# Kernel tuning notes

Measured on AMD Instinct MI355X. Metric: run time of the kernel, lower is better.

## Reference

```python
import jax, jax.numpy as jnp
import numpy as np

# ---- static problem configuration (matches init_kwargs) ----
N_PAIRS = 256
NODES_PER_GRAPH = 64
EDGES_PER_GRAPH = 200
MAX_EDGES = 256            # max_edge_set_size
N_GRAPHS = 2 * N_PAIRS     # query/corpus interleaved
N_NODES = N_GRAPHS * NODES_PER_GRAPH
N_EDGES = N_GRAPHS * EDGES_PER_GRAPH
NODE_DIM = 16
EDGE_DIM = 16
H = 128                    # node_state_dim
E_ENC = 64                 # encoded edge feature dim
MSG = 256                  # edge_hidden_sizes[-1] = 2*H (GMN GRU convention)
SK = 32                    # sinkhorn_feature_dim
PROP_STEPS = 5
SK_ITERS = 20
TEMP = 0.1


def setup_inputs() -> dict:
    key = jax.random.key(0)
    ks = jax.random.split(key, 16)
    node_features = jax.random.normal(ks[0], (N_NODES, NODE_DIM), jnp.float32)
    edge_features = jax.random.normal(ks[1], (N_EDGES, EDGE_DIM), jnp.float32)
    # edges are grouped per graph (graph g owns edges [g*E, (g+1)*E)) and
    # endpoints stay inside graph g's node range, as get_graph_features assumes
    offs = np.repeat(np.arange(N_GRAPHS) * NODES_PER_GRAPH, EDGES_PER_GRAPH)
    rng = np.random.default_rng(0)
    from_idx = jnp.asarray(offs + rng.integers(0, NODES_PER_GRAPH, N_EDGES), jnp.int32)
    to_idx = jnp.asarray(offs + rng.integers(0, NODES_PER_GRAPH, N_EDGES), jnp.int32)

    def lin(k, i, o):
        return jax.random.normal(k, (i, o), jnp.float32) / np.sqrt(i).astype(np.float32)

    p = dict(
        enc_node_w=lin(ks[2], NODE_DIM, H), enc_node_b=jnp.zeros((H,), jnp.float32),
        enc_edge_w=lin(ks[3], EDGE_DIM, E_ENC), enc_edge_b=jnp.zeros((E_ENC,), jnp.float32),
        msg_w1=lin(ks[4], 2 * H + E_ENC, MSG), msg_b1=jnp.zeros((MSG,), jnp.float32),
        msg_w2=lin(ks[5], MSG, MSG), msg_b2=jnp.zeros((MSG,), jnp.float32),
        rmsg_w1=lin(ks[6], 2 * H + E_ENC, MSG), rmsg_b1=jnp.zeros((MSG,), jnp.float32),
        rmsg_w2=lin(ks[7], MSG, MSG), rmsg_b2=jnp.zeros((MSG,), jnp.float32),
        gru_w_ih=lin(ks[8], MSG, 3 * H), gru_b_ih=jnp.zeros((3 * H,), jnp.float32),
        gru_w_hh=lin(ks[9], H, 3 * H), gru_b_hh=jnp.zeros((3 * H,), jnp.float32),
        sk_w1=lin(ks[10], MSG, SK), sk_b1=jnp.zeros((SK,), jnp.float32),
        sk_w2=lin(ks[11], SK, SK), sk_b2=jnp.zeros((SK,), jnp.float32),
    )
    return {"node_features": node_features, "edge_features": edge_features,
            "from_idx": from_idx, "to_idx": to_idx, **p}


def _mlp2(x, w1, b1, w2, b2):
    # Linear -> ReLU -> Linear (GMN MLP: no activation after last layer)
    return jax.nn.relu(x @ w1 + b1) @ w2 + b2


def reference(node_features, edge_features, from_idx, to_idx,
              enc_node_w, enc_node_b, enc_edge_w, enc_edge_b,
              msg_w1, msg_b1, msg_w2, msg_b2,
              rmsg_w1, rmsg_b1, rmsg_w2, rmsg_b2,
              gru_w_ih, gru_b_ih, gru_w_hh, gru_b_hh,
              sk_w1, sk_b1, sk_w2, sk_b2):
    # ---- GraphEncoder (single-layer MLPs) ----
    h = node_features @ enc_node_w + enc_node_b          # [N_NODES, H]
    e = edge_features @ enc_edge_w + enc_edge_b          # [N_EDGES, E_ENC]

    def edge_msgs(h):
        s, d = h[from_idx], h[to_idx]                    # gathers [N_EDGES, H]
        fwd = _mlp2(jnp.concatenate([s, d, e], axis=1), msg_w1, msg_b1, msg_w2, msg_b2)
        rev = _mlp2(jnp.concatenate([d, s, e], axis=1), rmsg_w1, rmsg_b1, rmsg_w2, rmsg_b2)
        return fwd, rev                                  # [N_EDGES, MSG] each

    # ---- propagation loop: gather -> edge MLP -> scatter -> GRU update ----
    for _ in range(PROP_STEPS):
        fwd, rev = edge_msgs(h)
        agg = (jax.ops.segment_sum(fwd, to_idx, num_segments=N_NODES)
               + jax.ops.segment_sum(rev, from_idx, num_segments=N_NODES))  # [N_NODES, MSG]
        gi = agg @ gru_w_ih + gru_b_ih                   # [N_NODES, 3H]
        gh = h @ gru_w_hh + gru_b_hh
        r = jax.nn.sigmoid(gi[:, :H] + gh[:, :H])
        z = jax.nn.sigmoid(gi[:, H:2 * H] + gh[:, H:2 * H])
        n = jnp.tanh(gi[:, 2 * H:] + r * gh[:, 2 * H:])
        h = (1.0 - z) * n + z * h                        # torch GRU update

    # ---- propagation_messages: per-edge fwd + rev message ----
    fwd, rev = edge_msgs(h)
    e_final = fwd + rev                                  # [N_EDGES, MSG]

    # ---- split_and_stack: per-graph edge sets padded to MAX_EDGES ----
    stacked = jnp.pad(e_final.reshape(N_GRAPHS, EDGES_PER_GRAPH, MSG),
                      ((0, 0), (0, MAX_EDGES - EDGES_PER_GRAPH), (0, 0)))
    q, c = stacked[0::2], stacked[1::2]                  # [B, MAX_EDGES, MSG]

    # ---- sinkhorn feature MLP + size mask ----
    tq = _mlp2(q, sk_w1, sk_b1, sk_w2, sk_b2)            # [B, MAX_EDGES, SK]
    tc = _mlp2(c, sk_w1, sk_b1, sk_w2, sk_b2)
    mask = (jnp.arange(MAX_EDGES) < EDGES_PER_GRAPH).astype(jnp.float32)[None, :, None]
    mq, mc = mask * tq, mask * tc

    # ---- log-domain Sinkhorn ----
    la = jnp.einsum('bif,bjf->bij', mq, mc) / TEMP       # [B, MAX_EDGES, MAX_EDGES]
    for _ in range(SK_ITERS):
        la = la - jax.nn.logsumexp(la, axis=2, keepdims=True)
        la = la - jax.nn.logsumexp(la, axis=1, keepdims=True)
    plan = jnp.exp(la)

    # ---- feature_alignment_score: -sum relu(q - P @ c) ----
    return -jnp.sum(jax.nn.relu(q - jnp.einsum('bij,bjf->bif', plan, c)), axis=(1, 2))
```

## Files before the change

kernel.cpp:

```cpp
#include <hip/hip_runtime.h>
#include <math.h>

typedef __attribute__((ext_vector_type(4))) float f32x4;
typedef __attribute__((ext_vector_type(8))) short s16x8;
typedef __attribute__((ext_vector_type(4))) short s16x4;

#define NN 32768
#define NE 102400
#define HD 128
#define EED 64
#define MSGD 256
#define NG 512
#define EPG 200
#define NP 256
#define SKD 32

__device__ inline short f2bf(float x){
  union{float f; unsigned u;} z; z.f=x;
  unsigned r = (z.u + 0x7fffu + ((z.u>>16)&1u)) >> 16;
  return (short)r;
}
__device__ inline float bf2f(unsigned short u){
  union{unsigned u; float f;} z; z.u = ((unsigned)u)<<16; return z.f;
}
__device__ inline float frcp(float x){
  float r; asm("v_rcp_f32 %0, %1" : "=v"(r) : "v"(x)); return r;
}

__global__ void __launch_bounds__(256) k_enc_node(const float* __restrict__ nf,
    const float* __restrict__ W, const float* __restrict__ b,
    float* __restrict__ h, short* __restrict__ hb){
  __shared__ float Ws[16*128];
  int t = threadIdx.x;
  for (int i=t;i<16*128;i+=256) Ws[i]=W[i];
  __syncthreads();
  int node = blockIdx.x*2 + (t>>7);
  int f = t & 127;
  const float* x = nf + node*16;
  float acc = b[f];
  #pragma unroll
  for (int k=0;k<16;k++) acc = fmaf(x[k], Ws[k*128+f], acc);
  h[node*HD+f] = acc;
  hb[node*HD+f] = f2bf(acc);
}

__global__ void __launch_bounds__(256) k_enc_edge(const float* __restrict__ ef,
    const float* __restrict__ W, const float* __restrict__ b, short* __restrict__ eeb){
  __shared__ float Ws[16*64];
  int t = threadIdx.x;
  for (int i=t;i<16*64;i+=256) Ws[i]=W[i];
  __syncthreads();
  int edge = blockIdx.x*4 + (t>>6);
  int f = t & 63;
  const float* x = ef + edge*16;
  float acc = b[f];
  #pragma unroll
  for (int k=0;k<16;k++) acc = fmaf(x[k], Ws[k*64+f], acc);
  eeb[edge*EED+f] = f2bf(acc);
}

__global__ void __launch_bounds__(256) k_pack(const float* __restrict__ W,
    short* __restrict__ dst, int K, int N){
  int NT = N >> 4;
  int i = blockIdx.x*256 + threadIdx.x;
  if (i >= (K/32)*NT*64) return;
  int l = i & 63, tile = i >> 6;
  int nt = tile % NT, kt = tile / NT;
  int lr = l & 15, lq = l >> 4;
  s16x8 v;
  #pragma unroll
  for (int j=0;j<8;j++)
    v[j] = f2bf(W[(size_t)(kt*32 + lq*8 + j)*N + nt*16 + lr]);
  *((s16x8*)dst + i) = v;
}

__global__ void __launch_bounds__(256) k_csr_count(const int* __restrict__ fidx,
    const int* __restrict__ tidx, int* __restrict__ cur_in, int* __restrict__ cur_out){
  int e = blockIdx.x*256 + threadIdx.x;
  if (e >= NE) return;
  atomicAdd(&cur_in[tidx[e]], 1);
  atomicAdd(&cur_out[fidx[e]], 1);
}
__global__ void k_csr_scan(int* __restrict__ cur_in, int* __restrict__ start_in,
    int* __restrict__ cur_out, int* __restrict__ start_out){
  if (threadIdx.x) return;
  int g = blockIdx.x;
  int n0 = g*64, base = g*EPG;
  int run = base;
  for (int i=0;i<64;i++){ int c=cur_in[n0+i]; start_in[n0+i]=run; cur_in[n0+i]=run; run+=c; }
  run = base;
  for (int i=0;i<64;i++){ int c=cur_out[n0+i]; start_out[n0+i]=run; cur_out[n0+i]=run; run+=c; }
}
__global__ void __launch_bounds__(256) k_csr_fill(const int* __restrict__ fidx,
    const int* __restrict__ tidx, int* __restrict__ cur_in, int* __restrict__ cur_out,
    int* __restrict__ list_in, int* __restrict__ list_out){
  int e = blockIdx.x*256 + threadIdx.x;
  if (e >= NE) return;
  int p1 = atomicAdd(&cur_in[tidx[e]], 1);  list_in[p1] = e;
  int p2 = atomicAdd(&cur_out[fidx[e]], 1); list_out[p2] = e;
}

__global__ void __launch_bounds__(256,2) k_msg_both(const short* __restrict__ hb,
    const short* __restrict__ eeb, const int* __restrict__ from_idx, const int* __restrict__ to_idx,
    const short* __restrict__ w1f, const float* __restrict__ b1f,
    const short* __restrict__ w2f, const float* __restrict__ b2f,
    const short* __restrict__ w1r, const float* __restrict__ b1r,
    const short* __restrict__ w2r, const float* __restrict__ b2r,
    short* __restrict__ mf, short* __restrict__ mr){
  __shared__ __align__(16) short Xs[64][328];
  __shared__ __align__(16) short Ys[64][264];
  __shared__ int sidx[64], didx[64];
  int t = threadIdx.x;
  int e0 = blockIdx.x*64;
  if (t < 64){ sidx[t]=from_idx[e0+t]; didx[t]=to_idx[e0+t]; }
  __syncthreads();
  for (int i=t; i<64*40; i+=256){
    int r = i/40, c8 = (i - r*40)*8;
    const short* src;
    if (c8 < 128)      src = hb + (size_t)sidx[r]*HD + c8;
    else if (c8 < 256) src = hb + (size_t)didx[r]*HD + (c8-128);
    else               src = eeb + (size_t)(e0+r)*EED + (c8-256);
    *(s16x8*)&Xs[r][c8] = *(const s16x8*)src;
  }
  __syncthreads();

  int wv = t>>6, l = t&63, lr = l&15, lq = l>>4;
  int cbase = wv*64;

  for (int dir=0; dir<2; dir++){
    const s16x8* W1v = (const s16x8*)(dir ? w1r : w1f);
    const float* B1  = dir ? b1r : b1f;
    const s16x8* W2v = (const s16x8*)(dir ? w2r : w2f);
    const float* B2  = dir ? b2r : b2f;

    f32x4 acc[4][4];
    #pragma unroll
    for (int ct=0; ct<4; ct++){
      float bb = B1[cbase + ct*16 + lr];
      #pragma unroll
      for (int rt=0; rt<4; rt++) acc[rt][ct] = (f32x4){bb,bb,bb,bb};
    }
    {
      s16x8 a0[4], b0[4], b1[4];
      int sc0 = dir ? 4 : 0;
      #pragma unroll
      for (int rt=0;rt<4;rt++) a0[rt] = *(const s16x8*)&Xs[rt*16+lr][sc0*32 + lq*8];
      #pragma unroll
      for (int ct=0;ct<4;ct++) b0[ct] = W1v[(size_t)(0*16 + wv*4 + ct)*64 + l];
      #pragma unroll
      for (int ct=0;ct<4;ct++) b1[ct] = W1v[(size_t)(1*16 + wv*4 + ct)*64 + l];
      #pragma unroll
      for (int kt=0; kt<10; kt++){
        s16x8 an[4], bn[4];
        if (kt < 9){
          int sc = (dir && (kt+1)<8) ? ((kt+1)^4) : (kt+1);
          #pragma unroll
          for (int rt=0;rt<4;rt++) an[rt] = *(const s16x8*)&Xs[rt*16+lr][sc*32 + lq*8];
        }
        if (kt < 8){
          #pragma unroll
          for (int ct=0;ct<4;ct++) bn[ct] = W1v[(size_t)((kt+2)*16 + wv*4 + ct)*64 + l];
        }
        #pragma unroll
        for (int rt=0; rt<4; rt++)
          #pragma unroll
          for (int ct=0; ct<4; ct++)
            acc[rt][ct] = __builtin_amdgcn_mfma_f32_16x16x32_bf16(a0[rt], b0[ct], acc[rt][ct], 0,0,0);
        #pragma unroll
        for (int i=0;i<4;i++){ a0[i]=an[i]; b0[i]=b1[i]; b1[i]=bn[i]; }
      }
    }
    #pragma unroll
    for (int rt=0; rt<4; rt++)
      #pragma unroll
      for (int ct=0; ct<4; ct++)
        #pragma unroll
        for (int r=0; r<4; r++)
          Ys[rt*16 + lq*4 + r][cbase + ct*16 + lr] = f2bf(fmaxf(acc[rt][ct][r], 0.f));
    __syncthreads();

    f32x4 acc2[4][4];
    #pragma unroll
    for (int ct=0; ct<4; ct++){
      float bb = B2[cbase + ct*16 + lr];
      #pragma unroll
      for (int rt=0; rt<4; rt++) acc2[rt][ct] = (f32x4){bb,bb,bb,bb};
    }
    {
      s16x8 a0[4], b0[4], b1[4];
      #pragma unroll
      for (int rt=0;rt<4;rt++) a0[rt] = *(const s16x8*)&Ys[rt*16+lr][lq*8];
      #pragma unroll
      for (int ct=0;ct<4;ct++) b0[ct] = W2v[(size_t)(0*16 + wv*4 + ct)*64 + l];
      #pragma unroll
      for (int ct=0;ct<4;ct++) b1[ct] = W2v[(size_t)(1*16 + wv*4 + ct)*64 + l];
      #pragma unroll
      for (int kt=0; kt<8; kt++){
        s16x8 an[4], bn[4];
        if (kt < 7){
          #pragma unroll
          for (int rt=0;rt<4;rt++) an[rt] = *(const s16x8*)&Ys[rt*16+lr][(kt+1)*32 + lq*8];
        }
        if (kt < 6){
          #pragma unroll
          for (int ct=0;ct<4;ct++) bn[ct] = W2v[(size_t)((kt+2)*16 + wv*4 + ct)*64 + l];
        }
        #pragma unroll
        for (int rt=0; rt<4; rt++)
          #pragma unroll
          for (int ct=0; ct<4; ct++)
            acc2[rt][ct] = __builtin_amdgcn_mfma_f32_16x16x32_bf16(a0[rt], b0[ct], acc2[rt][ct], 0,0,0);
        #pragma unroll
        for (int i=0;i<4;i++){ a0[i]=an[i]; b0[i]=b1[i]; b1[i]=bn[i]; }
      }
    }
    __syncthreads();
    #pragma unroll
    for (int rt=0; rt<4; rt++)
      #pragma unroll
      for (int ct=0; ct<4; ct++)
        #pragma unroll
        for (int r=0; r<4; r++)
          Ys[rt*16 + lq*4 + r][cbase + ct*16 + lr] = f2bf(acc2[rt][ct][r]);
    __syncthreads();
    {
      short* dst = (dir ? mr : mf) + (size_t)e0*MSGD;
      for (int i=t; i<64*32; i+=256){
        int row = i>>5, c8 = (i&31)*8;
        *(s16x8*)&dst[(size_t)row*MSGD + c8] = *(const s16x8*)&Ys[row][c8];
      }
    }
    __syncthreads();
  }
}

__global__ void __launch_bounds__(256) k_gather(const unsigned short* __restrict__ mf,
    const unsigned short* __restrict__ mr,
    const int* __restrict__ start_in, const int* __restrict__ end_in, const int* __restrict__ list_in,
    const int* __restrict__ start_out, const int* __restrict__ end_out, const int* __restrict__ list_out,
    short* __restrict__ aggb){
  int n = blockIdx.x*4 + (threadIdx.x>>6);
  int l = threadIdx.x & 63;
  float4 acc = {0.f,0.f,0.f,0.f};
  int s0 = start_in[n], e0 = end_in[n];
  for (int i=s0; i<e0; i++){
    int e = list_in[i];
    ushort4 v = *(const ushort4*)&mf[(size_t)e*MSGD + 4*l];
    acc.x += bf2f(v.x); acc.y += bf2f(v.y); acc.z += bf2f(v.z); acc.w += bf2f(v.w);
  }
  int s1 = start_out[n], e1 = end_out[n];
  for (int i=s1; i<e1; i++){
    int e = list_out[i];
    ushort4 v = *(const ushort4*)&mr[(size_t)e*MSGD + 4*l];
    acc.x += bf2f(v.x); acc.y += bf2f(v.y); acc.z += bf2f(v.z); acc.w += bf2f(v.w);
  }
  s16x4 o;
  o[0]=f2bf(acc.x); o[1]=f2bf(acc.y); o[2]=f2bf(acc.z); o[3]=f2bf(acc.w);
  *(s16x4*)&aggb[(size_t)n*MSGD + 4*l] = o;
}

__global__ void __launch_bounds__(256,2) k_msg_fin(const short* __restrict__ hb,
    const short* __restrict__ eeb, const int* __restrict__ from_idx, const int* __restrict__ to_idx,
    const short* __restrict__ w1f, const float* __restrict__ b1f,
    const short* __restrict__ w2f, const float* __restrict__ b2f,
    const short* __restrict__ w1r, const float* __restrict__ b1r,
    const short* __restrict__ w2r, const float* __restrict__ b2r,
    short* __restrict__ efb){
  __shared__ __align__(16) short Xs[64][328];
  __shared__ __align__(16) short Ys[64][264];
  __shared__ int sidx[64], didx[64];
  int t = threadIdx.x;
  int e0 = blockIdx.x*64;
  if (t < 64){ sidx[t]=from_idx[e0+t]; didx[t]=to_idx[e0+t]; }
  __syncthreads();
  for (int i=t; i<64*40; i+=256){
    int r = i/40, c8 = (i - r*40)*8;
    const short* src;
    if (c8 < 128)      src = hb + (size_t)sidx[r]*HD + c8;
    else if (c8 < 256) src = hb + (size_t)didx[r]*HD + (c8-128);
    else               src = eeb + (size_t)(e0+r)*EED + (c8-256);
    *(s16x8*)&Xs[r][c8] = *(const s16x8*)src;
  }
  __syncthreads();

  int wv = t>>6, l = t&63, lr = l&15, lq = l>>4;
  int cbase = wv*64;
  f32x4 fsv[4][4];

  for (int dir=0; dir<2; dir++){
    const s16x8* W1v = (const s16x8*)(dir ? w1r : w1f);
    const float* B1  = dir ? b1r : b1f;
    const s16x8* W2v = (const s16x8*)(dir ? w2r : w2f);
    const float* B2  = dir ? b2r : b2f;

    f32x4 acc[4][4];
    #pragma unroll
    for (int ct=0; ct<4; ct++){
      float bb = B1[cbase + ct*16 + lr];
      #pragma unroll
      for (int rt=0; rt<4; rt++) acc[rt][ct] = (f32x4){bb,bb,bb,bb};
    }
    {
      s16x8 a0[4], b0[4], b1[4];
      int sc0 = dir ? 4 : 0;
      #pragma unroll
      for (int rt=0;rt<4;rt++) a0[rt] = *(const s16x8*)&Xs[rt*16+lr][sc0*32 + lq*8];
      #pragma unroll
      for (int ct=0;ct<4;ct++) b0[ct] = W1v[(size_t)(0*16 + wv*4 + ct)*64 + l];
      #pragma unroll
      for (int ct=0;ct<4;ct++) b1[ct] = W1v[(size_t)(1*16 + wv*4 + ct)*64 + l];
      #pragma unroll
      for (int kt=0; kt<10; kt++){
        s16x8 an[4], bn[4];
        if (kt < 9){
          int sc = (dir && (kt+1)<8) ? ((kt+1)^4) : (kt+1);
          #pragma unroll
          for (int rt=0;rt<4;rt++) an[rt] = *(const s16x8*)&Xs[rt*16+lr][sc*32 + lq*8];
        }
        if (kt < 8){
          #pragma unroll
          for (int ct=0;ct<4;ct++) bn[ct] = W1v[(size_t)((kt+2)*16 + wv*4 + ct)*64 + l];
        }
        #pragma unroll
        for (int rt=0; rt<4; rt++)
          #pragma unroll
          for (int ct=0; ct<4; ct++)
            acc[rt][ct] = __builtin_amdgcn_mfma_f32_16x16x32_bf16(a0[rt], b0[ct], acc[rt][ct], 0,0,0);
        #pragma unroll
        for (int i=0;i<4;i++){ a0[i]=an[i]; b0[i]=b1[i]; b1[i]=bn[i]; }
      }
    }
    #pragma unroll
    for (int rt=0; rt<4; rt++)
      #pragma unroll
      for (int ct=0; ct<4; ct++)
        #pragma unroll
        for (int r=0; r<4; r++)
          Ys[rt*16 + lq*4 + r][cbase + ct*16 + lr] = f2bf(fmaxf(acc[rt][ct][r], 0.f));
    __syncthreads();

    f32x4 acc2[4][4];
    #pragma unroll
    for (int ct=0; ct<4; ct++){
      float bb = B2[cbase + ct*16 + lr];
      #pragma unroll
      for (int rt=0; rt<4; rt++) acc2[rt][ct] = (f32x4){bb,bb,bb,bb};
    }
    {
      s16x8 a0[4], b0[4], b1[4];
      #pragma unroll
      for (int rt=0;rt<4;rt++) a0[rt] = *(const s16x8*)&Ys[rt*16+lr][lq*8];
      #pragma unroll
      for (int ct=0;ct<4;ct++) b0[ct] = W2v[(size_t)(0*16 + wv*4 + ct)*64 + l];
      #pragma unroll
      for (int ct=0;ct<4;ct++) b1[ct] = W2v[(size_t)(1*16 + wv*4 + ct)*64 + l];
      #pragma unroll
      for (int kt=0; kt<8; kt++){
        s16x8 an[4], bn[4];
        if (kt < 7){
          #pragma unroll
          for (int rt=0;rt<4;rt++) an[rt] = *(const s16x8*)&Ys[rt*16+lr][(kt+1)*32 + lq*8];
        }
        if (kt < 6){
          #pragma unroll
          for (int ct=0;ct<4;ct++) bn[ct] = W2v[(size_t)((kt+2)*16 + wv*4 + ct)*64 + l];
        }
        #pragma unroll
        for (int rt=0; rt<4; rt++)
          #pragma unroll
          for (int ct=0; ct<4; ct++)
            acc2[rt][ct] = __builtin_amdgcn_mfma_f32_16x16x32_bf16(a0[rt], b0[ct], acc2[rt][ct], 0,0,0);
        #pragma unroll
        for (int i=0;i<4;i++){ a0[i]=an[i]; b0[i]=b1[i]; b1[i]=bn[i]; }
      }
    }

    if (dir==0){
      #pragma unroll
      for (int rt=0; rt<4; rt++)
        #pragma unroll
        for (int ct=0; ct<4; ct++) fsv[rt][ct] = acc2[rt][ct];
      __syncthreads();
    } else {
      __syncthreads();
      #pragma unroll
      for (int rt=0; rt<4; rt++)
        #pragma unroll
        for (int ct=0; ct<4; ct++)
          #pragma unroll
          for (int r=0; r<4; r++)
            Ys[rt*16 + lq*4 + r][cbase + ct*16 + lr] = f2bf(fsv[rt][ct][r] + acc2[rt][ct][r]);
      __syncthreads();
      short* dst = efb + (size_t)e0*MSGD;
      for (int i=t; i<64*32; i+=256){
        int row = i>>5, c8 = (i&31)*8;
        *(s16x8*)&dst[(size_t)row*MSGD + c8] = *(const s16x8*)&Ys[row][c8];
      }
    }
  }
}

__global__ void __launch_bounds__(256,2) k_gru(const float* __restrict__ h,
    const short* __restrict__ hb, const short* __restrict__ aggb,
    const short* __restrict__ wih_p, const float* __restrict__ bih,
    const short* __restrict__ whh_p, const float* __restrict__ bhh,
    float* __restrict__ hnew, short* __restrict__ hnewb){
  __shared__ __align__(16) short aggs[64][264];
  __shared__ __align__(16) short hs[64][136];
  int t = threadIdx.x;
  int n0 = blockIdx.x*64;
  for (int i=t; i<64*32; i+=256){
    int r = i>>5, c8 = (i&31)*8;
    *(s16x8*)&aggs[r][c8] = *(const s16x8*)&aggb[(size_t)(n0+r)*MSGD + c8];
  }
  for (int i=t; i<64*16; i+=256){
    int r = i>>4, c8 = (i&15)*8;
    *(s16x8*)&hs[r][c8] = *(const s16x8*)&hb[(size_t)(n0+r)*HD + c8];
  }
  __syncthreads();

  int wv = t>>6, l = t&63, lr = l&15, lq = l>>4;
  const s16x8* Wih_v = (const s16x8*)wih_p;
  const s16x8* Whh_v = (const s16x8*)whh_p;

  f32x4 gi[4][6], gh[4][6];
  #pragma unroll
  for (int ct=0; ct<6; ct++){
    int bcol = (ct>>1)*128 + wv*32 + (ct&1)*16 + lr;
    float bi = bih[bcol], bh = bhh[bcol];
    #pragma unroll
    for (int rt=0; rt<4; rt++){
      gi[rt][ct] = (f32x4){bi,bi,bi,bi};
      gh[rt][ct] = (f32x4){bh,bh,bh,bh};
    }
  }
  for (int kt=0; kt<8; kt++){
    s16x8 af[4], bfr[6];
    #pragma unroll
    for (int rt=0; rt<4; rt++) af[rt] = *(const s16x8*)&aggs[rt*16+lr][kt*32 + lq*8];
    #pragma unroll
    for (int ct=0; ct<6; ct++){
      int nt = (ct>>1)*8 + wv*2 + (ct&1);
      bfr[ct] = Wih_v[(size_t)(kt*24 + nt)*64 + l];
    }
    #pragma unroll
    for (int rt=0; rt<4; rt++)
      #pragma unroll
      for (int ct=0; ct<6; ct++)
        gi[rt][ct] = __builtin_amdgcn_mfma_f32_16x16x32_bf16(af[rt], bfr[ct], gi[rt][ct], 0,0,0);
  }
  for (int kt=0; kt<4; kt++){
    s16x8 af[4], bfr[6];
    #pragma unroll
    for (int rt=0; rt<4; rt++) af[rt] = *(const s16x8*)&hs[rt*16+lr][kt*32 + lq*8];
    #pragma unroll
    for (int ct=0; ct<6; ct++){
      int nt = (ct>>1)*8 + wv*2 + (ct&1);
      bfr[ct] = Whh_v[(size_t)(kt*24 + nt)*64 + l];
    }
    #pragma unroll
    for (int rt=0; rt<4; rt++)
      #pragma unroll
      for (int ct=0; ct<6; ct++)
        gh[rt][ct] = __builtin_amdgcn_mfma_f32_16x16x32_bf16(af[rt], bfr[ct], gh[rt][ct], 0,0,0);
  }
  #pragma unroll
  for (int rt=0; rt<4; rt++)
    #pragma unroll
    for (int j=0; j<2; j++)
      #pragma unroll
      for (int r=0; r<4; r++){
        int row = n0 + rt*16 + lq*4 + r;
        int col = wv*32 + j*16 + lr;
        float rr = 1.f/(1.f + __expf(-(gi[rt][j][r]   + gh[rt][j][r])));
        float zz = 1.f/(1.f + __expf(-(gi[rt][2+j][r] + gh[rt][2+j][r])));
        float gn = gi[rt][4+j][r] + rr*gh[rt][4+j][r];
        float nn = 1.f - 2.f/(__expf(2.f*gn) + 1.f);
        float hold = h[(size_t)row*HD + col];
        float hv = (1.f - zz)*nn + zz*hold;
        hnew[(size_t)row*HD + col] = hv;
        hnewb[(size_t)row*HD + col] = f2bf(hv);
      }
}

__global__ void __launch_bounds__(256,2) k_tall(const short* __restrict__ efb,
    const short* __restrict__ W1p, const float* __restrict__ b1,
    const short* __restrict__ W2p, const float* __restrict__ b2,
    float* __restrict__ tall){
  __shared__ __align__(16) short Xs[64][264];
  __shared__ __align__(16) short Ys[64][40];
  int t = threadIdx.x;
  int g = blockIdx.x>>2, r0 = (blockIdx.x&3)*64;
  for (int i=t; i<64*32; i+=256){
    int r = i>>5, c8 = (i&31)*8;
    int row = r0 + r;
    s16x8 v = (row < EPG) ? *(const s16x8*)&efb[((size_t)g*EPG + row)*MSGD + c8]
                          : (s16x8){0,0,0,0,0,0,0,0};
    *(s16x8*)&Xs[r][c8] = v;
  }
  __syncthreads();
  int wv = t>>6, l = t&63, lr = l&15, lq = l>>4;
  const s16x8* W1v = (const s16x8*)W1p;
  const s16x8* W2v = (const s16x8*)W2p;
  f32x4 acc[2];
  #pragma unroll
  for (int ct=0; ct<2; ct++){
    float bb = b1[ct*16 + lr];
    acc[ct] = (f32x4){bb,bb,bb,bb};
  }
  for (int kt=0; kt<8; kt++){
    s16x8 a = *(const s16x8*)&Xs[wv*16+lr][kt*32 + lq*8];
    #pragma unroll
    for (int ct=0; ct<2; ct++){
      s16x8 bfr = W1v[(size_t)(kt*2 + ct)*64 + l];
      acc[ct] = __builtin_amdgcn_mfma_f32_16x16x32_bf16(a, bfr, acc[ct], 0,0,0);
    }
  }
  #pragma unroll
  for (int ct=0; ct<2; ct++)
    #pragma unroll
    for (int r=0; r<4; r++)
      Ys[wv*16 + lq*4 + r][ct*16 + lr] = f2bf(fmaxf(acc[ct][r], 0.f));
  __syncthreads();
  f32x4 acc2[2];
  #pragma unroll
  for (int ct=0; ct<2; ct++){
    float bb = b2[ct*16 + lr];
    acc2[ct] = (f32x4){bb,bb,bb,bb};
  }
  {
    s16x8 a = *(const s16x8*)&Ys[wv*16+lr][lq*8];
    #pragma unroll
    for (int ct=0; ct<2; ct++){
      s16x8 bfr = W2v[(size_t)ct*64 + l];
      acc2[ct] = __builtin_amdgcn_mfma_f32_16x16x32_bf16(a, bfr, acc2[ct], 0,0,0);
    }
  }
  #pragma unroll
  for (int ct=0; ct<2; ct++)
    #pragma unroll
    for (int r=0; r<4; r++){
      int row = r0 + wv*16 + lq*4 + r;
      tall[((size_t)g*256 + row)*SKD + ct*16 + lr] = (row < EPG) ? acc2[ct][r] : 0.f;
    }
}

__global__ void __attribute__((amdgpu_waves_per_eu(4,4))) __launch_bounds__(1024)
k_sinkhorn(const float* __restrict__ tall, short* __restrict__ plan){
  __shared__ float tqs[256*32];
  __shared__ float tcsT[32*257];
  __shared__ float cv[256];
  __shared__ float psm[16][256];
  int p = blockIdx.x, t = threadIdx.x;
  int w = t>>6, l = t&63;
  int rbase = w*16;
  const float* tq = tall + (size_t)(2*p)*8192;
  const float* tc = tall + (size_t)(2*p+1)*8192;
  for (int i=t; i<8192; i+=1024){
    tqs[i] = tq[i];
    tcsT[(i&31)*257 + (i>>5)] = tc[i];
  }
  __syncthreads();
  float4 E[16];
  #pragma unroll
  for (int kg=0; kg<4; kg++){
    float4 a0_ = {0.f,0.f,0.f,0.f}, a1_ = a0_, a2_ = a0_, a3_ = a0_;
    for (int kk=0; kk<32; kk+=4){
      float4 c0 = *(const float4*)&tcsT[(kk+0)*257 + 4*l];
      float4 c1 = *(const float4*)&tcsT[(kk+1)*257 + 4*l];
      float4 c2 = *(const float4*)&tcsT[(kk+2)*257 + 4*l];
      float4 c3 = *(const float4*)&tcsT[(kk+3)*257 + 4*l];
      float4 q0 = *(const float4*)&tqs[(rbase+kg*4+0)*32 + kk];
      float4 q1 = *(const float4*)&tqs[(rbase+kg*4+1)*32 + kk];
      float4 q2 = *(const float4*)&tqs[(rbase+kg*4+2)*32 + kk];
      float4 q3 = *(const float4*)&tqs[(rbase+kg*4+3)*32 + kk];
      a0_.x = fmaf(q0.x,c0.x, fmaf(q0.y,c1.x, fmaf(q0.z,c2.x, fmaf(q0.w,c3.x, a0_.x))));
      a0_.y = fmaf(q0.x,c0.y, fmaf(q0.y,c1.y, fmaf(q0.z,c2.y, fmaf(q0.w,c3.y, a0_.y))));
      a0_.z = fmaf(q0.x,c0.z, fmaf(q0.y,c1.z, fmaf(q0.z,c2.z, fmaf(q0.w,c3.z, a0_.z))));
      a0_.w = fmaf(q0.x,c0.w, fmaf(q0.y,c1.w, fmaf(q0.z,c2.w, fmaf(q0.w,c3.w, a0_.w))));
      a1_.x = fmaf(q1.x,c0.x, fmaf(q1.y,c1.x, fmaf(q1.z,c2.x, fmaf(q1.w,c3.x, a1_.x))));
      a1_.y = fmaf(q1.x,c0.y, fmaf(q1.y,c1.y, fmaf(q1.z,c2.y, fmaf(q1.w,c3.y, a1_.y))));
      a1_.z = fmaf(q1.x,c0.z, fmaf(q1.y,c1.z, fmaf(q1.z,c2.z, fmaf(q1.w,c3.z, a1_.z))));
      a1_.w = fmaf(q1.x,c0.w, fmaf(q1.y,c1.w, fmaf(q1.z,c2.w, fmaf(q1.w,c3.w, a1_.w))));
      a2_.x = fmaf(q2.x,c0.x, fmaf(q2.y,c1.x, fmaf(q2.z,c2.x, fmaf(q2.w,c3.x, a2_.x))));
      a2_.y = fmaf(q2.x,c0.y, fmaf(q2.y,c1.y, fmaf(q2.z,c2.y, fmaf(q2.w,c3.y, a2_.y))));
      a2_.z = fmaf(q2.x,c0.z, fmaf(q2.y,c1.z, fmaf(q2.z,c2.z, fmaf(q2.w,c3.z, a2_.z))));
      a2_.w = fmaf(q2.x,c0.w, fmaf(q2.y,c1.w, fmaf(q2.z,c2.w, fmaf(q2.w,c3.w, a2_.w))));
      a3_.x = fmaf(q3.x,c0.x, fmaf(q3.y,c1.x, fmaf(q3.z,c2.x, fmaf(q3.w,c3.x, a3_.x))));
      a3_.y = fmaf(q3.x,c0.y, fmaf(q3.y,c1.y, fmaf(q3.z,c2.y, fmaf(q3.w,c3.y, a3_.y))));
      a3_.z = fmaf(q3.x,c0.z, fmaf(q3.y,c1.z, fmaf(q3.z,c2.z, fmaf(q3.w,c3.z, a3_.z))));
      a3_.w = fmaf(q3.x,c0.w, fmaf(q3.y,c1.w, fmaf(q3.z,c2.w, fmaf(q3.w,c3.w, a3_.w))));
    }
    #pragma unroll
    for (int j=0; j<4; j++){
      float4 a = (j==0)?a0_:(j==1)?a1_:(j==2)?a2_:a3_;
      a.x *= 10.f; a.y *= 10.f; a.z *= 10.f; a.w *= 10.f;
      float m = fmaxf(fmaxf(a.x,a.y), fmaxf(a.z,a.w));
      #pragma unroll
      for (int off=32; off; off>>=1) m = fmaxf(m, __shfl_xor(m, off));
      float s = __expf(a.x-m)+__expf(a.y-m)+__expf(a.z-m)+__expf(a.w-m);
      #pragma unroll
      for (int off=32; off; off>>=1) s += __shfl_xor(s, off);
      float r = m + __logf(s);
      E[kg*4+j].x = __expf(a.x - r); E[kg*4+j].y = __expf(a.y - r);
      E[kg*4+j].z = __expf(a.z - r); E[kg*4+j].w = __expf(a.w - r);
    }
  }

  for (int it=0; it<20; it++){
    float4 sm = {0.f,0.f,0.f,0.f};
    #pragma unroll
    for (int k=0;k<16;k++){
      sm.x += E[k].x; sm.y += E[k].y; sm.z += E[k].z; sm.w += E[k].w;
    }
    *(float4*)&psm[w][4*l] = sm;
    __syncthreads();
    if (t < 256){
      float s = psm[0][t];
      #pragma unroll
      for (int ww=1; ww<16; ww++) s += psm[ww][t];
      cv[t] = frcp(s);
    }
    __syncthreads();
    float4 ic = *(const float4*)&cv[4*l];
    #pragma unroll
    for (int k=0;k<16;k++){
      E[k].x *= ic.x; E[k].y *= ic.y; E[k].z *= ic.z; E[k].w *= ic.w;
    }
    if (it < 19){
      #pragma unroll
      for (int k=0;k<16;k++){
        float s = E[k].x + E[k].y + E[k].z + E[k].w;
        #pragma unroll
        for (int off=32; off; off>>=1) s += __shfl_xor(s, off);
        float inv = frcp(s);
        E[k].x *= inv; E[k].y *= inv; E[k].z *= inv; E[k].w *= inv;
      }
    }
  }
  short* P = plan + (size_t)p*65536;
  #pragma unroll
  for (int k=0;k<16;k++){
    s16x4 o;
    o[0]=f2bf(E[k].x); o[1]=f2bf(E[k].y); o[2]=f2bf(E[k].z); o[3]=f2bf(E[k].w);
    *(s16x4*)&P[(size_t)(rbase+k)*256 + 4*l] = o;
  }
}

__global__ void __launch_bounds__(256,2) k_loss(const short* __restrict__ plan,
    const short* __restrict__ efb, float* __restrict__ out){
  __shared__ __align__(16) short Ps[128][40];
  __shared__ __align__(16) short Cs[256][40];
  __shared__ float red[4];
  int t = threadIdx.x;
  int b = blockIdx.x, p = b>>1, rh = b&1;
  int i0 = rh*128;
  int wv = t>>6, l = t&63, lr = l&15, lq = l>>4;
  const short* Pb = plan + (size_t)p*65536;
  const unsigned short* C = (const unsigned short*)(efb + (size_t)(2*p+1)*EPG*MSGD);
  const unsigned short* Q = (const unsigned short*)(efb + (size_t)(2*p)*EPG*MSGD);

  f32x4 acc[2][16];
  #pragma unroll
  for (int rt=0;rt<2;rt++)
    #pragma unroll
    for (int ct=0;ct<16;ct++) acc[rt][ct] = (f32x4){0.f,0.f,0.f,0.f};

  for (int kt=0; kt<8; kt++){
    __syncthreads();
    for (int i=t; i<128*4; i+=256){
      int r = i>>2, c8 = (i&3)*8;
      *(s16x8*)&Ps[r][c8] = *(const s16x8*)&Pb[(size_t)(i0+r)*256 + kt*32 + c8];
    }
    for (int i=t; i<32*64; i+=256){
      int k = i>>6, c4 = (i&63)*4;
      int j = kt*32 + k;
      ushort4 v = (j < EPG) ? *(const ushort4*)&C[(size_t)j*256 + c4] : (ushort4){0,0,0,0};
      Cs[c4+0][k]=(short)v.x; Cs[c4+1][k]=(short)v.y; Cs[c4+2][k]=(short)v.z; Cs[c4+3][k]=(short)v.w;
    }
    __syncthreads();
    s16x8 a0 = *(const s16x8*)&Ps[wv*32      + lr][lq*8];
    s16x8 a1 = *(const s16x8*)&Ps[wv*32 + 16 + lr][lq*8];
    #pragma unroll
    for (int ct=0; ct<16; ct++){
      s16x8 bfr = *(const s16x8*)&Cs[ct*16+lr][lq*8];
      acc[0][ct] = __builtin_amdgcn_mfma_f32_16x16x32_bf16(a0, bfr, acc[0][ct], 0,0,0);
      acc[1][ct] = __builtin_amdgcn_mfma_f32_16x16x32_bf16(a1, bfr, acc[1][ct], 0,0,0);
    }
  }
  float s = 0.f;
  #pragma unroll
  for (int rt=0; rt<2; rt++)
    #pragma unroll
    for (int ct=0; ct<16; ct++)
      #pragma unroll
      for (int r=0; r<4; r++){
        int row = i0 + wv*32 + rt*16 + lq*4 + r;
        int col = ct*16 + lr;
        float q = (row < EPG) ? bf2f(Q[(size_t)row*256 + col]) : 0.f;
        s += fmaxf(q - acc[rt][ct][r], 0.f);
      }
  #pragma unroll
  for (int off=32; off; off>>=1) s += __shfl_xor(s, off);
  if (l==0) red[wv] = s;
  __syncthreads();
  if (t==0) atomicAdd(&out[p], -(red[0]+red[1]+red[2]+red[3]));
}

extern "C" void kernel_launch(void* const* d_in, const int* in_sizes, int n_in,
                              void* d_out, int out_size, void* d_ws, size_t ws_size,
                              hipStream_t stream){
  const float* nf   = (const float*)d_in[0];
  const float* ef   = (const float*)d_in[1];
  const int*   fidx = (const int*)d_in[2];
  const int*   tidx = (const int*)d_in[3];
  const float* enw  = (const float*)d_in[4];
  const float* enb  = (const float*)d_in[5];
  const float* eew  = (const float*)d_in[6];
  const float* eeb_w= (const float*)d_in[7];
  const float* mw1  = (const float*)d_in[8];
  const float* mb1  = (const float*)d_in[9];
  const float* mw2  = (const float*)d_in[10];
  const float* mb2  = (const float*)d_in[11];
  const float* rw1  = (const float*)d_in[12];
  const float* rb1  = (const float*)d_in[13];
  const float* rw2  = (const float*)d_in[14];
  const float* rb2  = (const float*)d_in[15];
  const float* wih  = (const float*)d_in[16];
  const float* bih  = (const float*)d_in[17];
  const float* whh  = (const float*)d_in[18];
  const float* bhh  = (const float*)d_in[19];
  const float* skw1 = (const float*)d_in[20];
  const float* skb1 = (const float*)d_in[21];
  const float* skw2 = (const float*)d_in[22];
  const float* skb2 = (const float*)d_in[23];
  float* out = (float*)d_out;

  float* ws = (float*)d_ws;
  float* h_a   = ws;
  float* h_b   = h_a + (size_t)NN*HD;
  short* hb_a  = (short*)(h_b + (size_t)NN*HD);
  short* hb_b  = hb_a + (size_t)NN*HD;
  short* ee_b  = hb_b + (size_t)NN*HD;
  short* mf    = ee_b + (size_t)NE*EED;
  short* mr    = mf + (size_t)NE*MSGD;
  short* e_finb = mf;
  float* t_all = (float*)(mr + (size_t)NE*MSGD);
  float* la    = t_all + (size_t)NG*256*SKD;

  short* w1f_p = (short*)t_all;
  short* w1r_p = w1f_p + 320*256;
  short* w2f_p = w1r_p + 320*256;
  short* w2r_p = w2f_p + 256*256;
  short* wih_p = w2r_p + 256*256;
  short* whh_p = wih_p + 256*384;
  int*   csr   = (int*)(t_all + 221184);
  int* cur_in    = csr;
  int* cur_out   = cur_in  + NN;
  int* start_in  = cur_out + NN;
  int* start_out = start_in + NN;
  int* list_in   = start_out + NN;
  int* list_out  = list_in + NE;

  short* aggb   = (short*)la;
  short* plan_s = (short*)la;
  short* skw1_p = (short*)(la + 9000000);
  short* skw2_p = skw1_p + 256*32;

  k_pack<<<40, 256, 0, stream>>>(mw1, w1f_p, 320, 256);
  k_pack<<<40, 256, 0, stream>>>(rw1, w1r_p, 320, 256);
  k_pack<<<32, 256, 0, stream>>>(mw2, w2f_p, 256, 256);
  k_pack<<<32, 256, 0, stream>>>(rw2, w2r_p, 256, 256);
  k_pack<<<48, 256, 0, stream>>>(wih, wih_p, 256, 384);
  k_pack<<<24, 256, 0, stream>>>(whh, whh_p, 128, 384);
  k_pack<<<4, 256, 0, stream>>>(skw1, skw1_p, 256, 32);
  k_pack<<<1, 256, 0, stream>>>(skw2, skw2_p, 32, 32);

  k_enc_node<<<NN/2, 256, 0, stream>>>(nf, enw, enb, h_a, hb_a);
  k_enc_edge<<<NE/4, 256, 0, stream>>>(ef, eew, eeb_w, ee_b);

  hipMemsetAsync(csr, 0, (size_t)2*NN*sizeof(int), stream);
  k_csr_count<<<NE/256, 256, 0, stream>>>(fidx, tidx, cur_in, cur_out);
  k_csr_scan<<<NG, 64, 0, stream>>>(cur_in, start_in, cur_out, start_out);
  k_csr_fill<<<NE/256, 256, 0, stream>>>(fidx, tidx, cur_in, cur_out, list_in, list_out);

  float* hc = h_a; float* hn = h_b;
  short* hbc = hb_a; short* hbn = hb_b;
  for (int step=0; step<5; step++){
    k_msg_both<<<NE/64, 256, 0, stream>>>(hbc, ee_b, fidx, tidx,
        w1f_p, mb1, w2f_p, mb2, w1r_p, rb1, w2r_p, rb2, mf, mr);
    k_gather<<<NN/4, 256, 0, stream>>>((const unsigned short*)mf, (const unsigned short*)mr,
        start_in, cur_in, list_in, start_out, cur_out, list_out, aggb);
    k_gru<<<NN/64, 256, 0, stream>>>(hc, hbc, aggb, wih_p, bih, whh_p, bhh, hn, hbn);
    float* tmp = hc; hc = hn; hn = tmp;
    short* tmb = hbc; hbc = hbn; hbn = tmb;
  }
  k_msg_fin<<<NE/64, 256, 0, stream>>>(hbc, ee_b, fidx, tidx,
      w1f_p, mb1, w2f_p, mb2, w1r_p, rb1, w2r_p, rb2, e_finb);

  k_tall<<<NG*4, 256, 0, stream>>>(e_finb, skw1_p, skb1, skw2_p, skb2, t_all);
  k_sinkhorn<<<NP, 1024, 0, stream>>>(t_all, plan_s);

  hipMemsetAsync(out, 0, (size_t)NP*sizeof(float), stream);
  k_loss<<<NP*2, 256, 0, stream>>>(plan_s, e_finb, out);
}
```

Baseline: 1.083 ms.

## Store message MLP output straight from registers and fuse weight-packing launches

The message kernel now writes its second-layer bf16 results directly from MFMA accumulators to global memory. It drops the LDS staging pass and two block barriers per tile, and adds one barrier on the reverse-direction path. The direct store permutes feature columns within each 64-column block, so the GRU input-weight packing permutes its K rows to match. The eight weight-packing launches are also merged into a single kernel. The risk is that any other consumer of the message buffers, such as the Sinkhorn feature MLP, sees permuted columns without matching weights, and the stores are narrower 8-byte writes.

```diff
diff --git a/kernel.cpp b/kernel.cpp
--- a/kernel.cpp
+++ b/kernel.cpp
@@ -59,18 +59,41 @@
   eeb[edge*EED+f] = f2bf(acc);
 }
 
-__global__ void __launch_bounds__(256) k_pack(const float* __restrict__ W,
-    short* __restrict__ dst, int K, int N){
+__global__ void __launch_bounds__(256) k_pack_all(
+    const float* __restrict__ mw1, const float* __restrict__ rw1,
+    const float* __restrict__ mw2, const float* __restrict__ rw2,
+    const float* __restrict__ wih, const float* __restrict__ whh,
+    const float* __restrict__ skw1, const float* __restrict__ skw2,
+    short* __restrict__ w1f_p, short* __restrict__ w1r_p,
+    short* __restrict__ w2f_p, short* __restrict__ w2r_p,
+    short* __restrict__ wih_p, short* __restrict__ whh_p,
+    short* __restrict__ skw1_p, short* __restrict__ skw2_p){
+  int b = blockIdx.x;
+  const float* W; short* dst; int K, N; int permK = 0;
+  if      (b < 40) { W=mw1;  dst=w1f_p;  K=320; N=256; }
+  else if (b < 80) { W=rw1;  dst=w1r_p;  K=320; N=256; b-=40; }
+  else if (b < 112){ W=mw2;  dst=w2f_p;  K=256; N=256; b-=80; }
+  else if (b < 144){ W=rw2;  dst=w2r_p;  K=256; N=256; b-=112; }
+  else if (b < 192){ W=wih;  dst=wih_p;  K=256; N=384; b-=144; permK=1; }
+  else if (b < 216){ W=whh;  dst=whh_p;  K=128; N=384; b-=192; }
+  else if (b < 220){ W=skw1; dst=skw1_p; K=256; N=32;  b-=216; }
+  else             { W=skw2; dst=skw2_p; K=32;  N=32;  b-=220; }
   int NT = N >> 4;
-  int i = blockIdx.x*256 + threadIdx.x;
+  int i = b*256 + (int)threadIdx.x;
   if (i >= (K/32)*NT*64) return;
   int l = i & 63, tile = i >> 6;
   int nt = tile % NT, kt = tile / NT;
   int lr = l & 15, lq = l >> 4;
   s16x8 v;
   #pragma unroll
-  for (int j=0;j<8;j++)
-    v[j] = f2bf(W[(size_t)(kt*32 + lq*8 + j)*N + nt*16 + lr]);
+  for (int j=0;j<8;j++){
+    int k = kt*32 + lq*8 + j;
+    if (permK){
+      int blk = k & ~63, w64 = k & 63;
+      k = blk + (w64 & 3)*16 + (w64 >> 2);
+    }
+    v[j] = f2bf(W[(size_t)k*N + nt*16 + lr]);
+  }
   *((s16x8*)dst + i) = v;
 }
 
@@ -170,6 +193,7 @@
         for (int i=0;i<4;i++){ a0[i]=an[i]; b0[i]=b1[i]; b1[i]=bn[i]; }
       }
     }
+    if (dir) __syncthreads();
     #pragma unroll
     for (int rt=0; rt<4; rt++)
       #pragma unroll
@@ -214,23 +238,19 @@
         for (int i=0;i<4;i++){ a0[i]=an[i]; b0[i]=b1[i]; b1[i]=bn[i]; }
       }
     }
-    __syncthreads();
-    #pragma unroll
-    for (int rt=0; rt<4; rt++)
-      #pragma unroll
-      for (int ct=0; ct<4; ct++)
-        #pragma unroll
-        for (int r=0; r<4; r++)
-          Ys[rt*16 + lq*4 + r][cbase + ct*16 + lr] = f2bf(acc2[rt][ct][r]);
-    __syncthreads();
     {
       short* dst = (dir ? mr : mf) + (size_t)e0*MSGD;
-      for (int i=t; i<64*32; i+=256){
-        int row = i>>5, c8 = (i&31)*8;
-        *(s16x8*)&dst[(size_t)row*MSGD + c8] = *(const s16x8*)&Ys[row][c8];
-      }
-    }
-    __syncthreads();
+      #pragma unroll
+      for (int rt=0; rt<4; rt++)
+        #pragma unroll
+        for (int r=0; r<4; r++){
+          int row = rt*16 + lq*4 + r;
+          s16x4 o;
+          #pragma unroll
+          for (int ct=0; ct<4; ct++) o[ct] = f2bf(acc2[rt][ct][r]);
+          *(s16x4*)&dst[(size_t)row*MSGD + cbase + lr*4] = o;
+        }
+    }
   }
 }
 
@@ -767,14 +787,8 @@
   short* skw1_p = (short*)(la + 9000000);
   short* skw2_p = skw1_p + 256*32;
 
-  k_pack<<<40, 256, 0, stream>>>(mw1, w1f_p, 320, 256);
-  k_pack<<<40, 256, 0, stream>>>(rw1, w1r_p, 320, 256);
-  k_pack<<<32, 256, 0, stream>>>(mw2, w2f_p, 256, 256);
-  k_pack<<<32, 256, 0, stream>>>(rw2, w2r_p, 256, 256);
-  k_pack<<<48, 256, 0, stream>>>(wih, wih_p, 256, 384);
-  k_pack<<<24, 256, 0, stream>>>(whh, whh_p, 128, 384);
-  k_pack<<<4, 256, 0, stream>>>(skw1, skw1_p, 256, 32);
-  k_pack<<<1, 256, 0, stream>>>(skw2, skw2_p, 32, 32);
+  k_pack_all<<<221, 256, 0, stream>>>(mw1, rw1, mw2, rw2, wih, whh, skw1, skw2,
+      w1f_p, w1r_p, w2f_p, w2r_p, wih_p, whh_p, skw1_p, skw2_p);
 
   k_enc_node<<<NN/2, 256, 0, stream>>>(nf, enw, enb, h_a, hb_a);
   k_enc_edge<<<NE/4, 256, 0, stream>>>(ef, eew, eeb_w, ee_b);
```

Result: slower. 1.128 ms (+4.2%).
